# Performance work log

Hardware: AMD Instinct MI355X
Metric: run time of the kernel (lower is better)

The kernel has to match this reference:

```python
import jax, jax.numpy as jnp
import numpy as np

IMG = 32        # imgSize
NU = 96         # n_units per grid axis
SHAPE = IMG * NU
ALPHA = 0.9     # running_variance_alpha
EPS_LR = 1e-07


def setup_inputs() -> dict:
    key = jax.random.key(0)
    k1, k2 = jax.random.split(key)
    x = jax.random.uniform(k1, (IMG, IMG), dtype=jnp.float32)
    som = jnp.clip(0.1 + 0.3 * jax.random.normal(k2, (SHAPE, SHAPE), dtype=jnp.float32), 0.0, 1.0)
    running_variance = jnp.ones((SHAPE, SHAPE), jnp.float32)
    radius = 48.0 * jnp.ones((NU, NU), jnp.float32)
    learning_rates = 0.5 * jnp.ones((NU, NU), jnp.float32)
    bmu_count = jnp.zeros((NU, NU, 10), jnp.float32)
    return {"x": x, "som": som, "running_variance": running_variance,
            "radius": radius, "learning_rates": learning_rates, "bmu_count": bmu_count}


def reference(x, som, running_variance, radius, learning_rates, bmu_count):
    # --- layer1: variance-weighted squared distance of input to every unit tile ---
    som_b = som.reshape(NU, IMG, NU, IMG).transpose(0, 2, 1, 3)            # [NU,NU,IMG,IMG]
    var_b = running_variance.reshape(NU, IMG, NU, IMG).transpose(0, 2, 1, 3)
    diff = som_b - x                                                        # broadcast input over grid
    z = jnp.sum(diff * diff / var_b, axis=(2, 3))                           # [NU,NU] feature map
    # --- layer2: BMU = argmin over the unit grid ---
    flat = jnp.argmin(z)
    bi = flat // NU
    bj = flat % NU
    input_matrix = jnp.tile(x, (NU, NU))                                    # [SHAPE,SHAPE]
    # --- create_mask: neighborhood-weighted codebook + EMA variance update ---
    r = radius[bi, bj]
    lr_b = learning_rates[bi, bj]
    dm = 1.0 / (2.0 * r * r)                                                # distance_modifier
    constant = -jnp.log(EPS_LR / lr_b) / dm
    ii = jnp.arange(NU, dtype=jnp.float32)
    bif = bi.astype(jnp.float32)
    bjf = bj.astype(jnp.float32)
    cart = jnp.sqrt((ii[:, None] - bif) ** 2 + (ii[None, :] - bjf) ** 2)    # cartesian_distances[:,:,bi,bj]
    modifier = jnp.where(cart > r, 0.0, cart)
    fm = learning_rates * jnp.exp(-modifier) * dm                           # [NU,NU]
    fm_full = jnp.repeat(jnp.repeat(fm, IMG, axis=1), IMG, axis=0)          # [SHAPE,SHAPE]
    va = jnp.clip(ALPHA - 0.5 + jax.nn.sigmoid(cart / constant), 0.0, 1.0)
    va_full = jnp.repeat(jnp.repeat(va, IMG, axis=1), IMG, axis=0)
    new_som = som + fm_full * (input_matrix - som)
    new_var = va_full * running_variance + (1.0 - va_full) * (input_matrix - new_som) ** 2
    new_som = jnp.clip(new_som, 0.0, 1.0)
    # --- decayRadius / decayLearningRate at the BMU (per-class counts -> class 0 used) ---
    new_radius = jnp.maximum(radius.at[bi, bj].set(jnp.exp(-bmu_count[bi, bj, 0] / 15.0)), 1e-05)
    new_lr = jnp.maximum(learning_rates.at[bi, bj].set(jnp.exp(-bmu_count[bi, bj, 0] / 25.0)), 1e-05)
    return new_som, new_var, new_radius, new_lr
```

## Files before the change

kernel.cpp:

```cpp
#include <hip/hip_runtime.h>
#include <math.h>

#define NU 96
#define IMG 32
#define SHAPE (NU * IMG)
#define NUNITS (NU * NU)
#define PLANE (SHAPE * SHAPE)
#define SHAPE4 (SHAPE / 4)
#define IMG4 (IMG / 4)
#define NSLOTS 64

typedef float vfloat4 __attribute__((ext_vector_type(4)));

__global__ __launch_bounds__(256) void zargmin_kernel(const float* __restrict__ x,
                                                      const float* __restrict__ som,
                                                      const float* __restrict__ var,
                                                      unsigned long long* __restrict__ slots) {
    const int v = blockIdx.x, u = blockIdx.y, t = threadIdx.x;
    const int i = t >> 3;
    const int jv = t & 7;

    const vfloat4* __restrict__ som4 = (const vfloat4*)som;
    const vfloat4* __restrict__ var4 = (const vfloat4*)var;
    const vfloat4* __restrict__ x4   = (const vfloat4*)x;

    const int idx = (u * IMG + i) * SHAPE4 + v * IMG4 + jv;
    const vfloat4 s  = som4[idx];
    const vfloat4 w  = var4[idx];
    const vfloat4 xx = x4[i * IMG4 + jv];

    const vfloat4 d = s - xx;
    const vfloat4 q = d * d / w;
    float p = q.x + q.y + q.z + q.w;

    #pragma unroll
    for (int off = 32; off > 0; off >>= 1) p += __shfl_down(p, off, 64);

    __shared__ float lds[4];
    const int wave = t >> 6, lane = t & 63;
    if (lane == 0) lds[wave] = p;
    __syncthreads();
    if (t == 0) {
        const float z = lds[0] + lds[1] + lds[2] + lds[3];
        const unsigned int flat = (unsigned int)(u * NU + v);
        const unsigned long long key =
            ((unsigned long long)__float_as_uint(z) << 32) | (unsigned long long)flat;
        atomicMin(&slots[flat & (NSLOTS - 1)], key);
    }
}

__global__ __launch_bounds__(256) void update_kernel(const float* __restrict__ x,
                                                     const float* __restrict__ som,
                                                     const float* __restrict__ var,
                                                     const float* __restrict__ radius,
                                                     const float* __restrict__ lrates,
                                                     const float* __restrict__ bmu_count,
                                                     const unsigned long long* __restrict__ slots,
                                                     float* __restrict__ out) {
    const int v = blockIdx.x, u = blockIdx.y, t = threadIdx.x;

    unsigned long long key = slots[t & 63];
    #pragma unroll
    for (int off = 32; off > 0; off >>= 1) {
        const unsigned long long o = __shfl_xor(key, off, 64);
        key = (o < key) ? o : key;
    }
    const int flat = (int)(key & 0xFFFFFFFFull);
    const int bi = flat / NU, bj = flat % NU;

    const float r    = radius[flat];
    const float lr_b = lrates[flat];
    const float dm   = 1.0f / (2.0f * r * r);
    const float constant = -logf(1e-7f / lr_b) / dm;

    const float du = (float)u - (float)bi;
    const float dv = (float)v - (float)bj;
    const float cart = sqrtf(du * du + dv * dv);
    const float modifier = (cart > r) ? 0.0f : cart;
    const float fm = lrates[u * NU + v] * expf(-modifier) * dm;
    const float sg = 1.0f / (1.0f + expf(-(cart / constant)));
    float va = 0.4f + sg;
    va = fminf(fmaxf(va, 0.0f), 1.0f);
    const float one_minus_va = 1.0f - va;

    const vfloat4* __restrict__ som4 = (const vfloat4*)som;
    const vfloat4* __restrict__ var4 = (const vfloat4*)var;
    const vfloat4* __restrict__ x4   = (const vfloat4*)x;
    vfloat4* __restrict__ out_som = (vfloat4*)out;
    vfloat4* __restrict__ out_var = (vfloat4*)(out + (size_t)PLANE);

    const int i = t >> 3, jv = t & 7;
    const int idx = (u * IMG + i) * SHAPE4 + v * IMG4 + jv;
    const vfloat4 s  = som4[idx];
    const vfloat4 w  = var4[idx];
    const vfloat4 xx = x4[i * IMG4 + jv];

    const vfloat4 n = s + fm * (xx - s);
    const vfloat4 d = xx - n;
    const vfloat4 nv = va * w + one_minus_va * d * d;
    vfloat4 ns;
    ns.x = fminf(fmaxf(n.x, 0.0f), 1.0f);
    ns.y = fminf(fmaxf(n.y, 0.0f), 1.0f);
    ns.z = fminf(fmaxf(n.z, 0.0f), 1.0f);
    ns.w = fminf(fmaxf(n.w, 0.0f), 1.0f);

    __builtin_nontemporal_store(ns, &out_som[idx]);
    __builtin_nontemporal_store(nv, &out_var[idx]);

    if (t == 0) {
        float* out_rad = out + 2 * (size_t)PLANE;
        float* out_lr  = out_rad + NUNITS;
        const int uv = u * NU + v;
        const float b0 = bmu_count[(size_t)flat * 10];
        const float rv = (uv == flat) ? expf(-b0 / 15.0f) : radius[uv];
        const float lv = (uv == flat) ? expf(-b0 / 25.0f) : lrates[uv];
        out_rad[uv] = fmaxf(rv, 1e-5f);
        out_lr[uv]  = fmaxf(lv, 1e-5f);
    }
}

extern "C" void kernel_launch(void* const* d_in, const int* in_sizes, int n_in,
                              void* d_out, int out_size, void* d_ws, size_t ws_size,
                              hipStream_t stream) {
    const float* x         = (const float*)d_in[0];
    const float* som       = (const float*)d_in[1];
    const float* var       = (const float*)d_in[2];
    const float* radius    = (const float*)d_in[3];
    const float* lrates    = (const float*)d_in[4];
    const float* bmu_count = (const float*)d_in[5];
    float* out = (float*)d_out;

    unsigned long long* slots = (unsigned long long*)d_ws;

    (void)hipMemsetAsync(slots, 0xFF, NSLOTS * sizeof(unsigned long long), stream);

    dim3 grid(NU, NU);
    zargmin_kernel<<<grid, 256, 0, stream>>>(x, som, var, slots);
    update_kernel<<<grid, 256, 0, stream>>>(x, som, var, radius, lrates, bmu_count, slots, out);
}
```

Before: 159.8 us.

## Fuse argmin and update into one cooperative kernel keeping tiles in registers

Result: slower. 241.9 us (+51.4%).

```diff
diff --git a/kernel.cpp b/kernel.cpp
--- a/kernel.cpp
+++ b/kernel.cpp
@@ -1,5 +1,8 @@
 #include <hip/hip_runtime.h>
+#include <hip/hip_cooperative_groups.h>
 #include <math.h>
+
+namespace cg = cooperative_groups;
 
 #define NU 96
 #define IMG 32
@@ -9,16 +12,121 @@
 #define SHAPE4 (SHAPE / 4)
 #define IMG4 (IMG / 4)
 #define NSLOTS 64
+#define NBLOCKS 1024
+#define TPB 9
 
 typedef float vfloat4 __attribute__((ext_vector_type(4)));
+
+__global__ __launch_bounds__(256, 4) void som_fused(const float* __restrict__ x,
+                                                    const float* __restrict__ som,
+                                                    const float* __restrict__ var,
+                                                    const float* __restrict__ radius,
+                                                    const float* __restrict__ lrates,
+                                                    const float* __restrict__ bmu_count,
+                                                    unsigned long long* __restrict__ slots,
+                                                    float* __restrict__ out) {
+    const int b = blockIdx.x, t = threadIdx.x;
+    const int i = t >> 3;
+    const int jv = t & 7;
+    const int wave = t >> 6, lane = t & 63;
+    const int tile0 = b * TPB;
+
+    const vfloat4* __restrict__ som4 = (const vfloat4*)som;
+    const vfloat4* __restrict__ var4 = (const vfloat4*)var;
+    const vfloat4* __restrict__ x4   = (const vfloat4*)x;
+
+    const vfloat4 xx = x4[i * IMG4 + jv];
+
+    vfloat4 s[TPB], w[TPB];
+    __shared__ float lds[TPB * 4];
+    #pragma unroll
+    for (int k = 0; k < TPB; k++) {
+        const int tile = tile0 + k;
+        const int u = tile / NU, v = tile - u * NU;
+        const int idx = (u * IMG + i) * SHAPE4 + v * IMG4 + jv;
+        s[k] = som4[idx];
+        w[k] = var4[idx];
+        const vfloat4 d = s[k] - xx;
+        const vfloat4 q = d * d / w[k];
+        float p = q.x + q.y + q.z + q.w;
+        #pragma unroll
+        for (int off = 32; off > 0; off >>= 1) p += __shfl_down(p, off, 64);
+        if (lane == 0) lds[k * 4 + wave] = p;
+    }
+    __syncthreads();
+    if (t < TPB) {
+        const float z = lds[t * 4] + lds[t * 4 + 1] + lds[t * 4 + 2] + lds[t * 4 + 3];
+        const unsigned int flat = (unsigned int)(tile0 + t);
+        const unsigned long long key =
+            ((unsigned long long)__float_as_uint(z) << 32) | (unsigned long long)flat;
+        atomicMin(&slots[flat & (NSLOTS - 1)], key);
+    }
+
+    cg::this_grid().sync();
+
+    unsigned long long key = slots[t & 63];
+    #pragma unroll
+    for (int off = 32; off > 0; off >>= 1) {
+        const unsigned long long o = __shfl_xor(key, off, 64);
+        key = (o < key) ? o : key;
+    }
+    const int flat = (int)(key & 0xFFFFFFFFull);
+    const int bi = flat / NU, bj = flat - bi * NU;
+
+    const float r    = radius[flat];
+    const float lr_b = lrates[flat];
+    const float dm   = 1.0f / (2.0f * r * r);
+    const float constant = -logf(1e-7f / lr_b) / dm;
+    const float b0 = bmu_count[(size_t)flat * 10];
+
+    vfloat4* __restrict__ out_som = (vfloat4*)out;
+    vfloat4* __restrict__ out_var = (vfloat4*)(out + (size_t)PLANE);
+    float* out_rad = out + 2 * (size_t)PLANE;
+    float* out_lr  = out_rad + NUNITS;
+
+    #pragma unroll
+    for (int k = 0; k < TPB; k++) {
+        const int tile = tile0 + k;
+        const int u = tile / NU, v = tile - u * NU;
+        const int idx = (u * IMG + i) * SHAPE4 + v * IMG4 + jv;
+
+        const float du = (float)u - (float)bi;
+        const float dv = (float)v - (float)bj;
+        const float cart = sqrtf(du * du + dv * dv);
+        const float modifier = (cart > r) ? 0.0f : cart;
+        const float fm = lrates[tile] * expf(-modifier) * dm;
+        const float sg = 1.0f / (1.0f + expf(-(cart / constant)));
+        float va = 0.4f + sg;
+        va = fminf(fmaxf(va, 0.0f), 1.0f);
+        const float one_minus_va = 1.0f - va;
+
+        const vfloat4 n = s[k] + fm * (xx - s[k]);
+        const vfloat4 d = xx - n;
+        const vfloat4 nv = va * w[k] + one_minus_va * d * d;
+        vfloat4 ns;
+        ns.x = fminf(fmaxf(n.x, 0.0f), 1.0f);
+        ns.y = fminf(fmaxf(n.y, 0.0f), 1.0f);
+        ns.z = fminf(fmaxf(n.z, 0.0f), 1.0f);
+        ns.w = fminf(fmaxf(n.w, 0.0f), 1.0f);
+
+        __builtin_nontemporal_store(ns, &out_som[idx]);
+        __builtin_nontemporal_store(nv, &out_var[idx]);
+
+        if (t == 0) {
+            const float rv = (tile == flat) ? expf(-b0 / 15.0f) : radius[tile];
+            const float lv = (tile == flat) ? expf(-b0 / 25.0f) : lrates[tile];
+            out_rad[tile] = fmaxf(rv, 1e-5f);
+            out_lr[tile]  = fmaxf(lv, 1e-5f);
+        }
+    }
+}
 
 __global__ __launch_bounds__(256) void zargmin_kernel(const float* __restrict__ x,
                                                       const float* __restrict__ som,
                                                       const float* __restrict__ var,
                                                       unsigned long long* __restrict__ slots) {
     const int v = blockIdx.x, u = blockIdx.y, t = threadIdx.x;
-    const int i = t >> 3;
-    const int jv = t & 7;
+    const int i = t >> 3, jv = t & 7;
 
     const vfloat4* __restrict__ som4 = (const vfloat4*)som;
     const vfloat4* __restrict__ var4 = (const vfloat4*)var;
@@ -32,7 +140,6 @@
     const vfloat4 d = s - xx;
     const vfloat4 q = d * d / w;
     float p = q.x + q.y + q.z + q.w;
-
     #pragma unroll
     for (int off = 32; off > 0; off >>= 1) p += __shfl_down(p, off, 64);
 
@@ -66,7 +173,7 @@
         key = (o < key) ? o : key;
     }
     const int flat = (int)(key & 0xFFFFFFFFull);
-    const int bi = flat / NU, bj = flat % NU;
+    const int bi = flat / NU, bj = flat - bi * NU;
 
     const float r    = radius[flat];
     const float lr_b = lrates[flat];
@@ -134,7 +241,14 @@
 
     (void)hipMemsetAsync(slots, 0xFF, NSLOTS * sizeof(unsigned long long), stream);
 
-    dim3 grid(NU, NU);
-    zargmin_kernel<<<grid, 256, 0, stream>>>(x, som, var, slots);
-    update_kernel<<<grid, 256, 0, stream>>>(x, som, var, radius, lrates, bmu_count, slots, out);
-}
+    void* args[] = { (void*)&x, (void*)&som, (void*)&var, (void*)&radius,
+                     (void*)&lrates, (void*)&bmu_count, (void*)&slots, (void*)&out };
+    hipError_t err = hipLaunchCooperativeKernel((const void*)som_fused, dim3(NBLOCKS),
+                                                dim3(256), args, 0, stream);
+    if (err != hipSuccess) {
+        dim3 grid(NU, NU);
+        zargmin_kernel<<<grid, 256, 0, stream>>>(x, som, var, slots);
+        update_kernel<<<grid, 256, 0, stream>>>(x, som, var, radius, lrates, bmu_count,
+                                                slots, out);
+    }
+}
```
